# Performance work log

Measured on AMD Instinct MI355X. Metric: run time of the kernel, lower is better.

The kernel has to match this reference:

```python
import jax, jax.numpy as jnp
import numpy as np

GROUPS = 32
EPS = 1e-6


def group_norm(x, scale, bias):
    b, h, w, c = x.shape
    xg = x.reshape(b, h, w, GROUPS, c // GROUPS)
    mean = xg.mean(axis=(1, 2, 4), keepdims=True)
    var = xg.var(axis=(1, 2, 4), keepdims=True)
    xg = (xg - mean) * jax.lax.rsqrt(var + EPS)
    return xg.reshape(b, h, w, c) * scale + bias


def setup_inputs() -> dict:
    key = jax.random.key(0)
    ks = jax.random.split(key, 8)
    b, h, w, c = 32, 32, 32, 512
    s = 1.0 / np.sqrt(c)
    return {
        "x": jax.random.normal(ks[0], (b, h, w, c), jnp.float32),
        "norm_scale": jnp.ones((c,), jnp.float32),
        "norm_bias": jnp.zeros((c,), jnp.float32),
        "wq": jax.random.normal(ks[1], (c, c), jnp.float32) * s,
        "bq": jnp.zeros((c,), jnp.float32),
        "wk": jax.random.normal(ks[2], (c, c), jnp.float32) * s,
        "bk": jnp.zeros((c,), jnp.float32),
        "wv": jax.random.normal(ks[3], (c, c), jnp.float32) * s,
        "bv": jnp.zeros((c,), jnp.float32),
        "wp": jax.random.normal(ks[4], (c, c), jnp.float32) * s,
        "bp": jnp.zeros((c,), jnp.float32),
    }


def reference(x, norm_scale, norm_bias, wq, bq, wk, bk, wv, bv, wp, bp):
    b, h, w, c = x.shape
    hn = group_norm(x, norm_scale, norm_bias)
    # 1x1 convs == per-pixel channel matmuls
    q = jnp.einsum('bhwc,cd->bhwd', hn, wq) + bq
    k = jnp.einsum('bhwc,cd->bhwd', hn, wk) + bk
    v = jnp.einsum('bhwc,cd->bhwd', hn, wv) + bv
    q = q.reshape(b, h * w, c)
    k = k.reshape(b, h * w, c)
    v = v.reshape(b, h * w, c)
    scores = jnp.einsum('bqc,bkc->bqk', q, k) * (c ** -0.5)  # [b, hw, hw]
    attn = jax.nn.softmax(scores, axis=-1)
    out = jnp.einsum('bqk,bkd->bqd', attn, v).reshape(b, h, w, c)
    out = jnp.einsum('bhwc,cd->bhwd', out, wp) + bp
    return x + out
```

## Files before the change

### kernel.cpp

```cpp
#include <hip/hip_runtime.h>
#include <stdint.h>
#include <stddef.h>


typedef short bh8 __attribute__((ext_vector_type(8)));
typedef __bf16 bf8 __attribute__((ext_vector_type(8)));
typedef float f4 __attribute__((ext_vector_type(4)));
typedef unsigned short u16;

#define NB 32
#define HW 1024
#define NC 512
#define NM (NB * HW)

__device__ __forceinline__ u16 f2bf(float f) {
    union { float f; uint32_t u; } v; v.f = f;
    uint32_t r = v.u + 0x7FFFu + ((v.u >> 16) & 1u);
    return (u16)(r >> 16);
}
__device__ __forceinline__ float bf2f(u16 h) {
    union { uint32_t u; float f; } v; v.u = ((uint32_t)h) << 16;
    return v.f;
}

using gas_p = const __attribute__((address_space(1))) void*;
using las_p = __attribute__((address_space(3))) void*;

__device__ __forceinline__ void async16(const void* g, void* l) {
    __builtin_amdgcn_global_load_lds((gas_p)g, (las_p)l, 16, 0, 0);
}

__device__ __forceinline__ f4 mfma16(bh8 a, bh8 b, f4 c) {
    return __builtin_amdgcn_mfma_f32_16x16x32_bf16(
        __builtin_bit_cast(bf8, a), __builtin_bit_cast(bf8, b), c, 0, 0, 0);
}

#define BAR()    __builtin_amdgcn_s_barrier()
#define SBAR()   __builtin_amdgcn_sched_barrier(0)
#define VMCNT(N) asm volatile("s_waitcnt vmcnt(" #N ")")

__global__ __launch_bounds__(256) void prep_kernel(
    const float* __restrict__ wq, const float* __restrict__ wk,
    const float* __restrict__ wv, const float* __restrict__ wp,
    u16* __restrict__ wT,
    const float* __restrict__ x, float2* __restrict__ part)
{
    const int bid = blockIdx.x;
    if (bid < 4096) {
        int idx = bid * 256 + threadIdx.x;
        int m = idx >> 18;
        int r = idx & 0x3FFFF;
        int k = r >> 9, n = r & 511;
        const float* w = (m == 0) ? wq : (m == 1) ? wk : (m == 2) ? wv : wp;
        wT[((size_t)m << 18) + (size_t)n * 512 + k] = f2bf(w[r]);
        return;
    }
    const int gb = bid - 4096;
    const int b = gb >> 3, s = gb & 7;
    const int t = threadIdx.x;
    const int c0 = (t & 127) * 4;
    const int pr = t >> 7;
    const float* xb = x + (size_t)b * HW * NC + (size_t)(s * 128) * NC + c0;
    float sum = 0.f, sq = 0.f;
#pragma unroll 8
    for (int i = 0; i < 64; ++i) {
        const float4 v = *(const float4*)(xb + (size_t)(pr + i * 2) * NC);
        sum += v.x + v.y + v.z + v.w;
        sq  += v.x * v.x + v.y * v.y + v.z * v.z + v.w * v.w;
    }
    __shared__ float2 red[256];
    red[t] = make_float2(sum, sq);
    __syncthreads();
    if (t < 32) {
        float S = 0.f, Q = 0.f;
#pragma unroll
        for (int p = 0; p < 2; ++p)
#pragma unroll
            for (int j = 0; j < 4; ++j) {
                const float2 v = red[t * 4 + j + p * 128];
                S += v.x; Q += v.y;
            }
        part[(size_t)gb * 32 + t] = make_float2(S, Q);
    }
}

__global__ __launch_bounds__(256) void gn_stats(
    const float2* __restrict__ part, float2* __restrict__ stats)
{
    const int p = blockIdx.x * 256 + threadIdx.x;
    const int b = p >> 5, g = p & 31;
    float S = 0.f, Q = 0.f;
#pragma unroll
    for (int s = 0; s < 8; ++s) {
        const float2 v = part[((size_t)(b * 8 + s)) * 32 + g];
        S += v.x; Q += v.y;
    }
    const float mean = S * (1.f / 16384.f);
    const float var = Q * (1.f / 16384.f) - mean * mean;
    stats[p] = make_float2(mean, rsqrtf(var + 1e-6f));
}

__global__ __launch_bounds__(256) void gn_apply(
    const float* __restrict__ x, const float2* __restrict__ stats,
    const float* __restrict__ scale, const float* __restrict__ bias,
    u16* __restrict__ hn)
{
    const size_t idx = (size_t)blockIdx.x * 256 + threadIdx.x;
    const size_t e = idx * 4;
    const int c0 = (int)(e & 511);
    const int bg = (int)(e >> 19) * 32 + (c0 >> 4);
    const float2 st = stats[bg];
    const float4 v = *(const float4*)(x + e);
    const float4 sc = *(const float4*)(scale + c0);
    const float4 bi = *(const float4*)(bias + c0);
    ushort4 o;
    o.x = f2bf((v.x - st.x) * st.y * sc.x + bi.x);
    o.y = f2bf((v.y - st.x) * st.y * sc.y + bi.y);
    o.z = f2bf((v.z - st.x) * st.y * sc.z + bi.z);
    o.w = f2bf((v.w - st.x) * st.y * sc.w + bi.w);
    *(ushort4*)(hn + e) = o;
}


template <int MAT, int Q>
__device__ __forceinline__ void stage_region(u16* ldsmat, const u16* g, int ldG,
                                             int w, int lane) {
#pragma unroll
    for (int j = 0; j < 2; ++j) {
        const int rowbase = (MAT == 0)
            ? (j * 128 + Q * 64 + w * 8)
            : ((j * 2 + (w >> 2)) * 64 + Q * 32 + (w & 3) * 8);
        const int row = rowbase + (lane >> 3);
        const int c16 = (lane & 7) ^ (lane >> 3);
        async16(g + (size_t)row * ldG + (c16 << 3), ldsmat + rowbase * 64);
    }
}

#define PHASE(P, D, QM, QN, LA, LB, SD, SMAT, SQ, SKT, GRD)                        \
    {                                                                              \
        if (LA) {                                                                  \
            _Pragma("unroll") for (int mt = 0; mt < 4; ++mt) {                     \
                const int arow = wm * 128 + (QM) * 64 + mt * 16 + r;               \
                _Pragma("unroll") for (int kk = 0; kk < 2; ++kk)                   \
                    paf[mt][kk] = *(const bh8*)&lds[D][0][arow * 64 +              \
                        (((kk * 4 + q4) ^ (r & 7)) << 3)];                         \
            }                                                                      \
        }                                                                          \
        if (LB) {                                                                  \
            _Pragma("unroll") for (int nt = 0; nt < 2; ++nt) {                     \
                const int brow = wn * 64 + (QN) * 32 + nt * 16 + r;                \
                _Pragma("unroll") for (int kk = 0; kk < 2; ++kk)                   \
                    pbf[nt][kk] = *(const bh8*)&lds[D][1][brow * 64 +              \
                        (((kk * 4 + q4) ^ (r & 7)) << 3)];                         \
            }                                                                      \
        }                                                                          \
        if (!(GRD) || it < NI - 1) {                                               \
            const size_t ko = (size_t)(2 * it + (SKT)) << 6;                       \
            if ((SMAT) == 0) stage_region<0, SQ>(&lds[SD][0][0], A_ + ko, K, wid, lane); \
            else             stage_region<1, SQ>(&lds[SD][1][0], B_ + ko, K, wid, lane); \
        }                                                                          \
        if (MB == 1) { BAR(); }                                                    \
        if (MB == 2) { SBAR(); }                                                   \
        __builtin_amdgcn_s_setprio(1);                                             \
        _Pragma("unroll") for (int mt = 0; mt < 4; ++mt)                           \
            _Pragma("unroll") for (int nt = 0; nt < 2; ++nt)                       \
                _Pragma("unroll") for (int kk = 0; kk < 2; ++kk)                   \
                    acc[(QM) * 4 + mt][(QN) * 2 + nt] =                            \
                        mfma16(paf[mt][kk], pbf[nt][kk],                           \
                               acc[(QM) * 4 + mt][(QN) * 2 + nt]);                 \
        __builtin_amdgcn_s_setprio(0);                                             \
        if ((P) == 3) { if (it < NI - 1) { VMCNT(4); } else { VMCNT(0); }          \
                        if (MB == 1) { SBAR(); } }                                 \
        if ((P) == 7) { VMCNT(4); if (MB == 1) { SBAR(); } }                       \
        BAR();                                                                     \
        if (MB != 1) { SBAR(); }                                                   \
    }

template <int MODE, int SWZ, int MB>
__global__ __launch_bounds__(512, 2) void gemm8(
    const u16* __restrict__ A, const u16* __restrict__ Bt,
    void* __restrict__ C0, void* __restrict__ C1,
    const float* __restrict__ b0, const float* __restrict__ b1,
    const float* __restrict__ b2, const float* __restrict__ resid,
    int K, int ldc, long strA, long strB, long strC, float alpha)
{
    __shared__ __align__(16) u16 lds[2][2][256 * 64];
    const int tid = threadIdx.x;
    const int wid = tid >> 6, lane = tid & 63;
    const int wm = wid >> 2, wn = wid & 3;
    const int r = lane & 15, q4 = lane >> 4;
    const int z = blockIdx.z;

    int m0, n0;
    if (SWZ > 0) {
        const int g = blockIdx.x;
        const int xcd = g & 7, s = g >> 3;
        const int mper = (int)(gridDim.x >> 3) / SWZ;
        m0 = (xcd * mper + s / SWZ) * 256;
        n0 = (s % SWZ) * 256;
    } else {
        m0 = blockIdx.y * 256;
        n0 = blockIdx.x * 256;
    }

    const u16* A_ = A + (size_t)z * strA + (size_t)m0 * K;
    const u16* B_ = Bt + (size_t)z * strB + (size_t)n0 * K;

    f4 acc[8][4];
#pragma unroll
    for (int ii = 0; ii < 8; ++ii)
#pragma unroll
        for (int jj = 0; jj < 4; ++jj) {
            f4 zr = {0.f, 0.f, 0.f, 0.f};
            acc[ii][jj] = zr;
        }
    bh8 paf[4][2], pbf[2][2];

    const int NI = K >> 7;

    stage_region<0, 0>(&lds[0][0][0], A_,      K, wid, lane);
    stage_region<1, 1>(&lds[0][1][0], B_,      K, wid, lane);
    stage_region<0, 1>(&lds[0][0][0], A_,      K, wid, lane);
    stage_region<1, 0>(&lds[0][1][0], B_,      K, wid, lane);
    stage_region<0, 0>(&lds[1][0][0], A_ + 64, K, wid, lane);
    stage_region<1, 1>(&lds[1][1][0], B_ + 64, K, wid, lane);
    VMCNT(4);
    if (MB == 1) { SBAR(); }
    BAR();
    if (MB != 1) { SBAR(); }

    for (int it = 0; it < NI; ++it) {
        PHASE(0, 0, 0, 0, 1, 1, 1, 0, 1, 1, 0)
        PHASE(1, 0, 0, 1, 0, 1, 1, 1, 0, 1, 0)
        PHASE(2, 0, 1, 1, 1, 0, 0, 0, 0, 2, 1)
        PHASE(3, 0, 1, 0, 0, 1, 0, 1, 1, 2, 1)
        PHASE(4, 1, 0, 0, 1, 1, 0, 0, 1, 2, 1)
        PHASE(5, 1, 0, 1, 0, 1, 0, 1, 0, 2, 1)
        PHASE(6, 1, 1, 1, 1, 0, 1, 0, 0, 3, 1)
        PHASE(7, 1, 1, 0, 0, 1, 1, 1, 1, 3, 1)
    }

#pragma unroll
    for (int am = 0; am < 8; ++am) {
#pragma unroll
        for (int an = 0; an < 4; ++an) {
            const int col = n0 + wn * 64 + an * 16 + r;
            const int row0 = m0 + wm * 128 + am * 16 + q4 * 4;
            if (MODE == 0) {
#pragma unroll
                for (int i2 = 0; i2 < 4; ++i2)
                    ((u16*)C0)[(size_t)z * strC + (size_t)(row0 + i2) * ldc + col] =
                        f2bf(acc[am][an][i2] * alpha);
            } else if (MODE == 3) {
                const float bv = b0[col];
#pragma unroll
                for (int i2 = 0; i2 < 4; ++i2) {
                    const size_t idx = (size_t)(row0 + i2) * ldc + col;
                    ((float*)C0)[idx] = acc[am][an][i2] + bv + resid[idx];
                }
            } else {
                const int seg = col >> 9, cl = col & 511;
                const float bv = (seg == 0 ? b0 : seg == 1 ? b1 : b2)[cl];
                if (seg < 2) {
                    u16* base = (u16*)C0 + (size_t)seg * (size_t)NM * 512;
#pragma unroll
                    for (int i2 = 0; i2 < 4; ++i2)
                        base[(size_t)(row0 + i2) * 512 + cl] = f2bf(acc[am][an][i2] + bv);
                } else {
                    const int bb = row0 >> 10, ml = row0 & 1023;
                    ushort4 o;
                    o.x = f2bf(acc[am][an][0] + bv);
                    o.y = f2bf(acc[am][an][1] + bv);
                    o.z = f2bf(acc[am][an][2] + bv);
                    o.w = f2bf(acc[am][an][3] + bv);
                    *(ushort4*)((u16*)C1 + ((size_t)(bb * 512 + cl)) * 1024 + ml) = o;
                }
            }
        }
    }
}

__global__ __launch_bounds__(256) void softmax_kernel(u16* __restrict__ s)
{
    const int wave = (blockIdx.x << 2) | (threadIdx.x >> 6);
    const int lane = threadIdx.x & 63;
    u16* rowp = s + (size_t)wave * 1024;

    float v[16];
#pragma unroll
    for (int c = 0; c < 4; ++c) {
        const ushort4 raw = *(const ushort4*)(rowp + c * 256 + lane * 4);
        v[c * 4 + 0] = bf2f(raw.x);
        v[c * 4 + 1] = bf2f(raw.y);
        v[c * 4 + 2] = bf2f(raw.z);
        v[c * 4 + 3] = bf2f(raw.w);
    }
    float m = -1e30f;
#pragma unroll
    for (int i = 0; i < 16; ++i) m = fmaxf(m, v[i]);
#pragma unroll
    for (int off = 32; off; off >>= 1) m = fmaxf(m, __shfl_xor(m, off));
    float sum = 0.f;
#pragma unroll
    for (int i = 0; i < 16; ++i) {
        v[i] = __expf(v[i] - m);
        sum += v[i];
    }
#pragma unroll
    for (int off = 32; off; off >>= 1) sum += __shfl_xor(sum, off);
    const float inv = 1.0f / sum;
#pragma unroll
    for (int c = 0; c < 4; ++c) {
        ushort4 o;
        o.x = f2bf(v[c * 4 + 0] * inv);
        o.y = f2bf(v[c * 4 + 1] * inv);
        o.z = f2bf(v[c * 4 + 2] * inv);
        o.w = f2bf(v[c * 4 + 3] * inv);
        *(ushort4*)(rowp + c * 256 + lane * 4) = o;
    }
}

extern "C" void kernel_launch(void* const* d_in, const int* in_sizes, int n_in,
                              void* d_out, int out_size, void* d_ws, size_t ws_size,
                              hipStream_t stream)
{
    (void)in_sizes; (void)n_in; (void)out_size; (void)ws_size;
    const float* x   = (const float*)d_in[0];
    const float* nsc = (const float*)d_in[1];
    const float* nbi = (const float*)d_in[2];
    const float* wq  = (const float*)d_in[3];
    const float* bq  = (const float*)d_in[4];
    const float* wk  = (const float*)d_in[5];
    const float* bk  = (const float*)d_in[6];
    const float* wv  = (const float*)d_in[7];
    const float* bv  = (const float*)d_in[8];
    const float* wp  = (const float*)d_in[9];
    const float* bp  = (const float*)d_in[10];
    float* out = (float*)d_out;

    char* ws = (char*)d_ws;
    u16* qb = (u16*)(ws);
    u16* kb = (u16*)(ws + (32ull << 20));
    u16* vT = (u16*)(ws + (64ull << 20));
    u16* sb = (u16*)(ws + (96ull << 20));
    u16* hn = (u16*)(ws + (160ull << 20));
    u16* ao = hn;
    u16* wT = (u16*)(ws + (192ull << 20));
    float2* gnp = (float2*)sb;
    float2* gns = (float2*)(ws + (97ull << 20));

    prep_kernel<<<4352, 256, 0, stream>>>(wq, wk, wv, wp, wT, x, gnp);
    gn_stats<<<4, 256, 0, stream>>>(gnp, gns);
    gn_apply<<<16384, 256, 0, stream>>>(x, gns, nsc, nbi, hn);

    const dim3 blk(512);
    gemm8<4, 6, 2><<<768, blk, 0, stream>>>(hn, wT, qb, vT, bq, bk, bv, nullptr,
                                            512, 512, 0, 0, 0, 1.f);

    const dim3 g2(4, 4, 32);
    gemm8<0, 0, 0><<<g2, blk, 0, stream>>>(qb, kb, sb, nullptr, nullptr, nullptr, nullptr, nullptr,
                                           512, 1024, 1024L * 512, 1024L * 512, 1024L * 1024,
                                           0.04419417382415922f);
    softmax_kernel<<<8192, dim3(256), 0, stream>>>(sb);

    const dim3 g3(2, 4, 32);
    gemm8<0, 0, 0><<<g3, blk, 0, stream>>>(sb, vT, ao, nullptr, nullptr, nullptr, nullptr, nullptr,
                                           1024, 512, 1024L * 1024, 512L * 1024, 1024L * 512,
                                           1.f);

    gemm8<3, 2, 0><<<256, blk, 0, stream>>>(ao, wT + 3 * 262144, out, nullptr, bp, nullptr, nullptr, x,
                                            512, 512, 0, 0, 0, 1.f);
}
```

Before: 377.7 us.

## Make GEMM blocks loop over multiple N tiles with cross-tile prefetch

The GEMM kernel becomes persistent along N: each block computes NT consecutive 256-wide output tiles, reusing the same A rows and prefetching the next tile's B slab during the last K iteration of the current tile. The QKV projection now launches 256 blocks with three tiles each, and the QK^T GEMM launches half as many blocks with two tiles each. This is meant to cut grid size to roughly one wave per CU, amortize prologue and launch overhead, and keep the pipeline full across tile boundaries. The cost is fewer blocks in flight, serialized epilogues inside each block, and removal of the MB==1 barrier variant.

Result: slower. 424.7 us (+12.4%).

```diff
diff --git a/kernel.cpp b/kernel.cpp
--- a/kernel.cpp
+++ b/kernel.cpp
@@ -136,7 +136,7 @@
     }
 }
 
-#define PHASE(P, D, QM, QN, LA, LB, SD, SMAT, SQ, SKT, GRD)                        \
+#define PHASE(P, D, QM, QN, LA, LB, SD, SMAT, SQ, SKT)                             \
     {                                                                              \
         if (LA) {                                                                  \
             _Pragma("unroll") for (int mt = 0; mt < 4; ++mt) {                     \
@@ -154,12 +154,21 @@
                         (((kk * 4 + q4) ^ (r & 7)) << 3)];                         \
             }                                                                      \
         }                                                                          \
-        if (!(GRD) || it < NI - 1) {                                               \
-            const size_t ko = (size_t)(2 * it + (SKT)) << 6;                       \
-            if ((SMAT) == 0) stage_region<0, SQ>(&lds[SD][0][0], A_ + ko, K, wid, lane); \
-            else             stage_region<1, SQ>(&lds[SD][1][0], B_ + ko, K, wid, lane); \
+        {                                                                          \
+            const int knext = 2 * it + (SKT);                                      \
+            if (knext < 2 * NI || t < NT - 1) {                                    \
+                const int kw = (knext < 2 * NI) ? knext : knext - 2 * NI;          \
+                if ((SMAT) == 0) {                                                 \
+                    stage_region<0, SQ>(&lds[SD][0][0],                            \
+                        A_ + ((size_t)kw << 6), K, wid, lane);                     \
+                } else {                                                           \
+                    const int tt = (knext < 2 * NI) ? t : t + 1;                   \
+                    const u16* Bs = Bz + (size_t)(np * NT + tt) * nstride +        \
+                                    ((size_t)kw << 6);                             \
+                    stage_region<1, SQ>(&lds[SD][1][0], Bs, K, wid, lane);         \
+                }                                                                  \
+            }                                                                      \
         }                                                                          \
-        if (MB == 1) { BAR(); }                                                    \
         if (MB == 2) { SBAR(); }                                                   \
         __builtin_amdgcn_s_setprio(1);                                             \
         _Pragma("unroll") for (int mt = 0; mt < 4; ++mt)                           \
@@ -169,14 +178,15 @@
                         mfma16(paf[mt][kk], pbf[nt][kk],                           \
                                acc[(QM) * 4 + mt][(QN) * 2 + nt]);                 \
         __builtin_amdgcn_s_setprio(0);                                             \
-        if ((P) == 3) { if (it < NI - 1) { VMCNT(4); } else { VMCNT(0); }          \
-                        if (MB == 1) { SBAR(); } }                                 \
-        if ((P) == 7) { VMCNT(4); if (MB == 1) { SBAR(); } }                       \
+        if ((P) == 3) {                                                            \
+            if (it == NI - 1 && t == NT - 1) { VMCNT(0); } else { VMCNT(4); }      \
+        }                                                                          \
+        if ((P) == 7) { VMCNT(4); }                                                \
         BAR();                                                                     \
-        if (MB != 1) { SBAR(); }                                                   \
-    }
-
-template <int MODE, int SWZ, int MB>
+        SBAR();                                                                    \
+    }
+
+template <int MODE, int SWZ, int MB, int NT, int NPAIR>
 __global__ __launch_bounds__(512, 2) void gemm8(
     const u16* __restrict__ A, const u16* __restrict__ Bt,
     void* __restrict__ C0, void* __restrict__ C1,
@@ -191,20 +201,21 @@
     const int r = lane & 15, q4 = lane >> 4;
     const int z = blockIdx.z;
 
-    int m0, n0;
+    int m0, np;
     if (SWZ > 0) {
         const int g = blockIdx.x;
         const int xcd = g & 7, s = g >> 3;
-        const int mper = (int)(gridDim.x >> 3) / SWZ;
-        m0 = (xcd * mper + s / SWZ) * 256;
-        n0 = (s % SWZ) * 256;
+        const int mper = (int)(gridDim.x >> 3) / NPAIR;
+        m0 = (xcd * mper + s / NPAIR) * 256;
+        np = s % NPAIR;
     } else {
+        np = blockIdx.x;
         m0 = blockIdx.y * 256;
-        n0 = blockIdx.x * 256;
     }
 
     const u16* A_ = A + (size_t)z * strA + (size_t)m0 * K;
-    const u16* B_ = Bt + (size_t)z * strB + (size_t)n0 * K;
+    const u16* Bz = Bt + (size_t)z * strB;
+    const size_t nstride = (size_t)256 * K;
 
     f4 acc[8][4];
 #pragma unroll
@@ -218,64 +229,80 @@
 
     const int NI = K >> 7;
 
-    stage_region<0, 0>(&lds[0][0][0], A_,      K, wid, lane);
-    stage_region<1, 1>(&lds[0][1][0], B_,      K, wid, lane);
-    stage_region<0, 1>(&lds[0][0][0], A_,      K, wid, lane);
-    stage_region<1, 0>(&lds[0][1][0], B_,      K, wid, lane);
-    stage_region<0, 0>(&lds[1][0][0], A_ + 64, K, wid, lane);
-    stage_region<1, 1>(&lds[1][1][0], B_ + 64, K, wid, lane);
+    {
+        const u16* B0 = Bz + (size_t)(np * NT) * nstride;
+        stage_region<0, 0>(&lds[0][0][0], A_,      K, wid, lane);
+        stage_region<1, 1>(&lds[0][1][0], B0,      K, wid, lane);
+        stage_region<0, 1>(&lds[0][0][0], A_,      K, wid, lane);
+        stage_region<1, 0>(&lds[0][1][0], B0,      K, wid, lane);
+        stage_region<0, 0>(&lds[1][0][0], A_ + 64, K, wid, lane);
+        stage_region<1, 1>(&lds[1][1][0], B0 + 64, K, wid, lane);
+    }
     VMCNT(4);
-    if (MB == 1) { SBAR(); }
     BAR();
-    if (MB != 1) { SBAR(); }
-
-    for (int it = 0; it < NI; ++it) {
-        PHASE(0, 0, 0, 0, 1, 1, 1, 0, 1, 1, 0)
-        PHASE(1, 0, 0, 1, 0, 1, 1, 1, 0, 1, 0)
-        PHASE(2, 0, 1, 1, 1, 0, 0, 0, 0, 2, 1)
-        PHASE(3, 0, 1, 0, 0, 1, 0, 1, 1, 2, 1)
-        PHASE(4, 1, 0, 0, 1, 1, 0, 0, 1, 2, 1)
-        PHASE(5, 1, 0, 1, 0, 1, 0, 1, 0, 2, 1)
-        PHASE(6, 1, 1, 1, 1, 0, 1, 0, 0, 3, 1)
-        PHASE(7, 1, 1, 0, 0, 1, 1, 1, 1, 3, 1)
-    }
-
-#pragma unroll
-    for (int am = 0; am < 8; ++am) {
-#pragma unroll
-        for (int an = 0; an < 4; ++an) {
-            const int col = n0 + wn * 64 + an * 16 + r;
-            const int row0 = m0 + wm * 128 + am * 16 + q4 * 4;
-            if (MODE == 0) {
-#pragma unroll
-                for (int i2 = 0; i2 < 4; ++i2)
-                    ((u16*)C0)[(size_t)z * strC + (size_t)(row0 + i2) * ldc + col] =
-                        f2bf(acc[am][an][i2] * alpha);
-            } else if (MODE == 3) {
-                const float bv = b0[col];
-#pragma unroll
-                for (int i2 = 0; i2 < 4; ++i2) {
-                    const size_t idx = (size_t)(row0 + i2) * ldc + col;
-                    ((float*)C0)[idx] = acc[am][an][i2] + bv + resid[idx];
-                }
-            } else {
-                const int seg = col >> 9, cl = col & 511;
-                const float bv = (seg == 0 ? b0 : seg == 1 ? b1 : b2)[cl];
-                if (seg < 2) {
-                    u16* base = (u16*)C0 + (size_t)seg * (size_t)NM * 512;
+    SBAR();
+
+#pragma unroll 1
+    for (int t = 0; t < NT; ++t) {
+        const int n0_t = (np * NT + t) * 256;
+#pragma unroll 1
+        for (int it = 0; it < NI; ++it) {
+            PHASE(0, 0, 0, 0, 1, 1, 1, 0, 1, 1)
+            PHASE(1, 0, 0, 1, 0, 1, 1, 1, 0, 1)
+            PHASE(2, 0, 1, 1, 1, 0, 0, 0, 0, 2)
+            PHASE(3, 0, 1, 0, 0, 1, 0, 1, 1, 2)
+            PHASE(4, 1, 0, 0, 1, 1, 0, 0, 1, 2)
+            PHASE(5, 1, 0, 1, 0, 1, 0, 1, 0, 2)
+            PHASE(6, 1, 1, 1, 1, 0, 1, 0, 0, 3)
+            PHASE(7, 1, 1, 0, 0, 1, 1, 1, 1, 3)
+        }
+
+#pragma unroll
+        for (int am = 0; am < 8; ++am) {
+#pragma unroll
+            for (int an = 0; an < 4; ++an) {
+                const int col = n0_t + wn * 64 + an * 16 + r;
+                const int row0 = m0 + wm * 128 + am * 16 + q4 * 4;
+                if (MODE == 0) {
 #pragma unroll
                     for (int i2 = 0; i2 < 4; ++i2)
-                        base[(size_t)(row0 + i2) * 512 + cl] = f2bf(acc[am][an][i2] + bv);
+                        ((u16*)C0)[(size_t)z * strC + (size_t)(row0 + i2) * ldc + col] =
+                            f2bf(acc[am][an][i2] * alpha);
+                } else if (MODE == 3) {
+                    const float bv = b0[col];
+#pragma unroll
+                    for (int i2 = 0; i2 < 4; ++i2) {
+                        const size_t idx = (size_t)(row0 + i2) * ldc + col;
+                        ((float*)C0)[idx] = acc[am][an][i2] + bv + resid[idx];
+                    }
                 } else {
-                    const int bb = row0 >> 10, ml = row0 & 1023;
-                    ushort4 o;
-                    o.x = f2bf(acc[am][an][0] + bv);
-                    o.y = f2bf(acc[am][an][1] + bv);
-                    o.z = f2bf(acc[am][an][2] + bv);
-                    o.w = f2bf(acc[am][an][3] + bv);
-                    *(ushort4*)((u16*)C1 + ((size_t)(bb * 512 + cl)) * 1024 + ml) = o;
+                    const int seg = col >> 9, cl = col & 511;
+                    const float bv = (seg == 0 ? b0 : seg == 1 ? b1 : b2)[cl];
+                    if (seg < 2) {
+                        u16* base = (u16*)C0 + (size_t)seg * (size_t)NM * 512;
+#pragma unroll
+                        for (int i2 = 0; i2 < 4; ++i2)
+                            base[(size_t)(row0 + i2) * 512 + cl] = f2bf(acc[am][an][i2] + bv);
+                    } else {
+                        const int bb = row0 >> 10, ml = row0 & 1023;
+                        ushort4 o;
+                        o.x = f2bf(acc[am][an][0] + bv);
+                        o.y = f2bf(acc[am][an][1] + bv);
+                        o.z = f2bf(acc[am][an][2] + bv);
+                        o.w = f2bf(acc[am][an][3] + bv);
+                        *(ushort4*)((u16*)C1 + ((size_t)(bb * 512 + cl)) * 1024 + ml) = o;
+                    }
                 }
             }
+        }
+        if (t < NT - 1) {
+#pragma unroll
+            for (int ii = 0; ii < 8; ++ii)
+#pragma unroll
+                for (int jj = 0; jj < 4; ++jj) {
+                    f4 zr = {0.f, 0.f, 0.f, 0.f};
+                    acc[ii][jj] = zr;
+                }
         }
     }
 }
@@ -354,20 +381,20 @@
     gn_apply<<<16384, 256, 0, stream>>>(x, gns, nsc, nbi, hn);
 
     const dim3 blk(512);
-    gemm8<4, 6, 2><<<768, blk, 0, stream>>>(hn, wT, qb, vT, bq, bk, bv, nullptr,
-                                            512, 512, 0, 0, 0, 1.f);
-
-    const dim3 g2(4, 4, 32);
-    gemm8<0, 0, 0><<<g2, blk, 0, stream>>>(qb, kb, sb, nullptr, nullptr, nullptr, nullptr, nullptr,
-                                           512, 1024, 1024L * 512, 1024L * 512, 1024L * 1024,
-                                           0.04419417382415922f);
+    gemm8<4, 1, 2, 3, 2><<<256, blk, 0, stream>>>(hn, wT, qb, vT, bq, bk, bv, nullptr,
+                                                  512, 512, 0, 0, 0, 1.f);
+
+    gemm8<0, 0, 0, 2, 2><<<dim3(2, 4, 32), blk, 0, stream>>>(
+        qb, kb, sb, nullptr, nullptr, nullptr, nullptr, nullptr,
+        512, 1024, 1024L * 512, 1024L * 512, 1024L * 1024,
+        0.04419417382415922f);
     softmax_kernel<<<8192, dim3(256), 0, stream>>>(sb);
 
-    const dim3 g3(2, 4, 32);
-    gemm8<0, 0, 0><<<g3, blk, 0, stream>>>(sb, vT, ao, nullptr, nullptr, nullptr, nullptr, nullptr,
-                                           1024, 512, 1024L * 1024, 512L * 1024, 1024L * 512,
-                                           1.f);
-
-    gemm8<3, 2, 0><<<256, blk, 0, stream>>>(ao, wT + 3 * 262144, out, nullptr, bp, nullptr, nullptr, x,
-                                            512, 512, 0, 0, 0, 1.f);
-}
+    gemm8<0, 0, 0, 1, 2><<<dim3(2, 4, 32), blk, 0, stream>>>(
+        sb, vT, ao, nullptr, nullptr, nullptr, nullptr, nullptr,
+        1024, 512, 1024L * 1024, 512L * 1024, 1024L * 512, 1.f);
+
+    gemm8<3, 1, 0, 1, 2><<<256, blk, 0, stream>>>(ao, wT + 3 * 262144, out, nullptr, bp,
+                                                  nullptr, nullptr, x,
+                                                  512, 512, 0, 0, 0, 1.f);
+}
```
